# Performance work log

Measured on AMD Instinct MI355X. Metric: run time of the kernel, lower is better.

The kernel has to match this reference:

```python
import jax, jax.numpy as jnp
import numpy as np

N, E, MUL, NZ, NR = 8192, 65536, 64, 10, 8
SQ3 = 3.0 ** 0.5
SQ2 = 2.0 ** 0.5


def _mlp(x, ws):
    # e3nn FullyConnectedNet: no biases, 1/sqrt(fan_in) scaling, silu on hidden layers
    for i, w in enumerate(ws):
        x = x @ w / jnp.sqrt(jnp.float32(w.shape[0]))
        if i < len(ws) - 1:
            x = jax.nn.silu(x)
    return x


def setup_inputs() -> dict:
    key = jax.random.key(0)
    ks = jax.random.split(key, 20)
    g = lambda i, sh: jax.random.normal(ks[i], sh, dtype=jnp.float32)
    return dict(
        node_attrs=jax.random.uniform(ks[0], (N, NZ), dtype=jnp.float32),
        node_feats=g(1, (N, MUL * 4)),            # 64x0e + 64x1o
        edge_attrs=g(2, (E, 4)),                  # SH: 1x0e + 1x1o
        edge_feats=g(3, (E, NR)),                 # radial basis
        edge_index=jax.random.randint(ks[4], (2, E), 0, N),
        magmom_node_inv_feats=g(5, (N, NR)),
        magmom_node_attrs=g(6, (N, 4)),           # 1x0e + 1x1o
        W_up_s=g(7, (MUL, MUL)), W_up_v=g(8, (MUL, MUL)),
        rmlp_w0=g(9, (2 * NR, 64)), rmlp_w1=g(10, (64, 64)),
        rmlp_w2=g(11, (64, 64)), rmlp_w3=g(12, (64, 5 * MUL)),
        mag_w=g(13, (2 * NR, 13 * MUL)),
        dens_w=g(14, (NR, 1)),
        lin_s_w=g(15, (5 * MUL, MUL)), lin_v_w=g(16, (8 * MUL, MUL)),
        skip_w_s=g(17, (MUL, NZ, MUL)), skip_w_v=g(18, (MUL, NZ, MUL)),
    )


def reference(node_attrs, node_feats, edge_attrs, edge_feats, edge_index,
              magmom_node_inv_feats, magmom_node_attrs,
              W_up_s, W_up_v, rmlp_w0, rmlp_w1, rmlp_w2, rmlp_w3,
              mag_w, dens_w, lin_s_w, lin_v_w, skip_w_s, skip_w_v):
    sender, receiver = edge_index[0], edge_index[1]
    num_nodes = node_feats.shape[0]
    mul = W_up_s.shape[0]

    # linear_up (per-l channel mixing)
    s = node_feats[:, :mul]
    v = node_feats[:, mul:].reshape(num_nodes, mul, 3)
    s = (s @ W_up_s) / jnp.sqrt(jnp.float32(mul))
    v = jnp.einsum('nui,uw->nwi', v, W_up_v) / jnp.sqrt(jnp.float32(mul))

    # radial weights conditioned on edge feats + sender magmom invariants
    efm = jnp.concatenate([edge_feats, magmom_node_inv_feats[sender]], axis=-1)
    tp_w = _mlp(efm, [rmlp_w0, rmlp_w1, rmlp_w2, rmlp_w3]).reshape(-1, 5, mul)
    wm = (efm @ mag_w / jnp.sqrt(jnp.float32(mag_w.shape[0]))).reshape(-1, 13, mul)
    edge_density = jnp.tanh((edge_feats @ dens_w / jnp.sqrt(jnp.float32(NR))) ** 2)  # [E,1]

    # conv_tp: node_feats[sender] x edge SH, uvu with per-edge weights (5 paths)
    xs, xv = s[sender], v[sender]          # [E,mul], [E,mul,3]
    y0, y1 = edge_attrs[:, :1], edge_attrs[:, 1:]
    m_s0 = tp_w[:, 0] * xs * y0                                       # 0e x 0e -> 0e
    m_v0 = tp_w[:, 1, :, None] * xs[:, :, None] * y1[:, None, :]      # 0e x 1o -> 1o
    m_v1 = tp_w[:, 2, :, None] * xv * y0[:, :, None]                  # 1o x 0e -> 1o
    m_s1 = tp_w[:, 3] * jnp.einsum('eui,ei->eu', xv, y1) / SQ3        # 1o x 1o -> 0e
    m_v2 = tp_w[:, 4, :, None] * jnp.cross(xv, y1[:, None, :]) / SQ2  # 1o x 1o -> 1e

    # magmom_conv_tp: mji x magmom_node_attrs[sender], uvu (13 paths)
    ma = magmom_node_attrs[sender]
    m0, m1 = ma[:, :1], ma[:, 1:]
    out_s, out_v = [], []
    p = 0
    for ss in (m_s0, m_s1):
        out_s.append(wm[:, p] * ss * m0); p += 1
        out_v.append(wm[:, p, :, None] * ss[:, :, None] * m1[:, None, :]); p += 1
    for vv in (m_v0, m_v1, m_v2):
        out_v.append(wm[:, p, :, None] * vv * m0[:, :, None]); p += 1
        out_s.append(wm[:, p] * jnp.einsum('eui,ei->eu', vv, m1) / SQ3); p += 1
        out_v.append(wm[:, p, :, None] * jnp.cross(vv, m1[:, None, :]) / SQ2); p += 1
    mm_s = jnp.stack(out_s, axis=1)   # [E,5,mul]
    mm_v = jnp.stack(out_v, axis=1)   # [E,8,mul,3]

    # scatter-sum to receivers
    density = jax.ops.segment_sum(edge_density, receiver, num_segments=num_nodes)  # [N,1]
    ms = jax.ops.segment_sum(mm_s, receiver, num_segments=num_nodes)               # [N,5,mul]
    mv = jax.ops.segment_sum(mm_v, receiver, num_segments=num_nodes)               # [N,8,mul,3]

    # magmom_linear + density normalization
    ms = ms.reshape(num_nodes, 5 * mul) @ lin_s_w / jnp.sqrt(jnp.float32(5 * mul))
    mv = jnp.einsum('nui,uw->nwi', mv.reshape(num_nodes, 8 * mul, 3), lin_v_w) / jnp.sqrt(jnp.float32(8 * mul))
    ms = ms / (density + 1.0)
    mv = mv / (density[:, :, None] + 1.0)

    # skip FullyConnectedTensorProduct with scalar node_attrs (species one-hot)
    fan = jnp.sqrt(jnp.float32(skip_w_s.shape[0] * skip_w_s.shape[1]))
    o_s = jnp.einsum('nu,nv,uvw->nw', ms, node_attrs, skip_w_s) / fan
    o_v = jnp.einsum('nui,nv,uvw->nwi', mv, node_attrs, skip_w_v) / fan

    # reshape_irreps: [N, mul, 1+3]
    return jnp.concatenate([o_s[:, :, None], o_v], axis=-1)
```

## Files before the change

### kernel.cpp

```cpp
#include <hip/hip_runtime.h>
#include <hip/hip_bf16.h>

#define NN 8192
#define EE 65536

typedef unsigned short u16;
typedef __attribute__((ext_vector_type(8))) short bf16x8;
typedef __attribute__((ext_vector_type(8))) unsigned short u16x8;
typedef __attribute__((ext_vector_type(4))) float f32x4;

#define OFF_W0    0
#define OFF_W1    2048
#define OFF_W2    6144
#define OFF_W3M   10240
#define OFF_MAGB  59392
#define OFF_MAGC  75776
#define OFF_LINS  79872
#define OFF_LINV  100352
#define OFF_SKS   133120
#define OFF_SKV   174080
#define WT_TOTAL  215040

__device__ __forceinline__ u16 f2bf(float f) {
  __hip_bfloat16 h = __float2bfloat16(f);
  return *reinterpret_cast<u16*>(&h);
}
__device__ __forceinline__ float bf2f(u16 v) {
  union { unsigned int u; float f; } x; x.u = ((unsigned int)v) << 16; return x.f;
}
__device__ __forceinline__ void split2(float x, u16& h, u16& l) {
  __hip_bfloat16 bh = __float2bfloat16(x);
  h = *reinterpret_cast<u16*>(&bh);
  float r = x - __bfloat162float(bh);
  __hip_bfloat16 bl = __float2bfloat16(r);
  l = *reinterpret_cast<u16*>(&bl);
}

#define MFMA(a, b, c) __builtin_amdgcn_mfma_f32_16x16x32_bf16((a), (b), (c), 0, 0, 0)

__global__ __launch_bounds__(256, 4) void k_edge(
    const u16* __restrict__ efm_h, const u16* __restrict__ efm_l,
    const u16* __restrict__ wt_h, const u16* __restrict__ wt_l,
    u16* __restrict__ cmbA, u16* __restrict__ cmbB, u16* __restrict__ cmbC)
{
  __shared__ u16 Hh[64 * 72], Hl[64 * 72];
  __shared__ u16 Bs[2][3072];
  __shared__ u16 Ct[64 * 80];
  const int tid  = threadIdx.x;
  const size_t pos0 = (size_t)blockIdx.x * 64;
  const int wave = tid >> 6, lane = tid & 63;
  const int quad = lane >> 4, lrow = lane & 15;
  const int kbase = quad * 8;
  const int rw = wave * 16;

  bf16x8 eah = {}, eal = {};
  if (quad < 2) {
    eah = *reinterpret_cast<const bf16x8*>(&efm_h[(pos0 + rw + lrow) * 16 + kbase]);
    eal = *reinterpret_cast<const bf16x8*>(&efm_l[(pos0 + rw + lrow) * 16 + kbase]);
  }

  {
    #pragma unroll
    for (int nt = 0; nt < 4; ++nt) {
      const size_t bo = (size_t)nt * 512 + lane * 8;
      const bf16x8 fbh = *reinterpret_cast<const bf16x8*>(wt_h + OFF_W0 + bo);
      const bf16x8 fbl = *reinterpret_cast<const bf16x8*>(wt_l + OFF_W0 + bo);
      f32x4 acc = {};
      acc = MFMA(eah, fbh, acc); acc = MFMA(eah, fbl, acc); acc = MFMA(eal, fbh, acc);
      #pragma unroll
      for (int r = 0; r < 4; ++r) {
        float t = acc[r];
        t = t / (1.0f + __expf(-t));
        u16 hh, ll; split2(t, hh, ll);
        const int row = rw + quad * 4 + r, col = nt * 16 + lrow;
        Hh[row * 72 + col] = hh; Hl[row * 72 + col] = ll;
      }
    }
  }

  #pragma unroll
  for (int layer = 0; layer < 2; ++layer) {
    const int OFF = layer ? OFF_W2 : OFF_W1;
    bf16x8 fah[2], fal[2];
    #pragma unroll
    for (int ks = 0; ks < 2; ++ks) {
      fah[ks] = *reinterpret_cast<const bf16x8*>(&Hh[(rw + lrow) * 72 + ks * 32 + kbase]);
      fal[ks] = *reinterpret_cast<const bf16x8*>(&Hl[(rw + lrow) * 72 + ks * 32 + kbase]);
    }
    f32x4 acc[4] = {};
    #pragma unroll
    for (int nt = 0; nt < 4; ++nt)
      #pragma unroll
      for (int ks = 0; ks < 2; ++ks) {
        const size_t bo = (size_t)(nt * 2 + ks) * 512 + lane * 8;
        const bf16x8 fbh = *reinterpret_cast<const bf16x8*>(wt_h + OFF + bo);
        const bf16x8 fbl = *reinterpret_cast<const bf16x8*>(wt_l + OFF + bo);
        acc[nt] = MFMA(fah[ks], fbh, acc[nt]);
        acc[nt] = MFMA(fah[ks], fbl, acc[nt]);
        acc[nt] = MFMA(fal[ks], fbh, acc[nt]);
      }
    #pragma unroll
    for (int nt = 0; nt < 4; ++nt)
      #pragma unroll
      for (int r = 0; r < 4; ++r) {
        float t = acc[nt][r];
        t = t / (1.0f + __expf(-t));
        u16 hh, ll; split2(t, hh, ll);
        const int row = rw + quad * 4 + r, col = nt * 16 + lrow;
        Hh[row * 72 + col] = hh; Hl[row * 72 + col] = ll;
      }
  }

  {
    bf16x8 fah[3], fal[3];
    #pragma unroll
    for (int ks = 0; ks < 2; ++ks) {
      fah[ks] = *reinterpret_cast<const bf16x8*>(&Hh[(rw + lrow) * 72 + ks * 32 + kbase]);
      fal[ks] = *reinterpret_cast<const bf16x8*>(&Hl[(rw + lrow) * 72 + ks * 32 + kbase]);
    }
    fah[2] = eah; fal[2] = eal;

    auto STAGE_A = [&](int s, int buf) {
      const size_t src = (size_t)OFF_W3M + (size_t)s * 1536;
      #pragma unroll
      for (int i = 0; i < 2; ++i) {
        const int idx = tid + i * 256;
        if (idx < 384) {
          const int b = (idx >= 192);
          const int off = (idx - (b ? 192 : 0)) * 8;
          *reinterpret_cast<uint4*>(&Bs[buf][(b ? 1536 : 0) + off]) =
              *reinterpret_cast<const uint4*>((b ? wt_l : wt_h) + src + off);
        }
      }
    };

    STAGE_A(0, 0);
    for (int s = 0; s < 32; ++s) {
      __syncthreads();
      if (s + 1 < 32) STAGE_A(s + 1, (s + 1) & 1);
      const int nt = s & 3;
      f32x4 acc = {};
      #pragma unroll
      for (int ks = 0; ks < 3; ++ks) {
        const bf16x8 bh = *reinterpret_cast<const bf16x8*>(&Bs[s & 1][ks * 512 + lane * 8]);
        const bf16x8 bl = *reinterpret_cast<const bf16x8*>(&Bs[s & 1][1536 + ks * 512 + lane * 8]);
        acc = MFMA(fah[ks], bh, acc); acc = MFMA(fah[ks], bl, acc); acc = MFMA(fal[ks], bh, acc);
      }
      #pragma unroll
      for (int r = 0; r < 4; ++r)
        Ct[(rw + quad * 4 + r) * 80 + ((nt * 16 + lrow) ^ (quad << 4))] = f2bf(acc[r]);
      if (nt == 3) {
        u16* dstA = cmbA + (size_t)(s >> 2) * ((size_t)EE * 64);
        #pragma unroll
        for (int i = 0; i < 2; ++i) {
          const int idx = lane + i * 64;
          const int rl = idx >> 3, c2 = idx & 7;
          const uint4 v4 = *reinterpret_cast<const uint4*>(
              &Ct[(rw + rl) * 80 + ((c2 * 8) ^ (((rl >> 2) & 3) << 4))]);
          *reinterpret_cast<uint4*>(&dstA[(pos0 + rw + rl) * 64 + c2 * 8]) = v4;
        }
      }
    }
  }

  {
    auto STAGE_B = [&](int t, int buf) {
      const size_t src = (size_t)OFF_MAGB + (size_t)t * 512;
      if (tid < 128) {
        const int b = (tid >= 64);
        const int off = (tid - (b ? 64 : 0)) * 8;
        *reinterpret_cast<uint4*>(&Bs[buf][(b ? 1536 : 0) + off]) =
            *reinterpret_cast<const uint4*>((b ? wt_l : wt_h) + src + off);
      }
    };

    STAGE_B(0, 0);
    for (int t = 0; t < 40; ++t) {
      __syncthreads();
      if (t + 1 < 40) STAGE_B(t + 1, (t + 1) & 1);
      const int nt = t & 3;
      const bf16x8 bh = *reinterpret_cast<const bf16x8*>(&Bs[t & 1][lane * 8]);
      const bf16x8 bl = *reinterpret_cast<const bf16x8*>(&Bs[t & 1][1536 + lane * 8]);
      f32x4 acc = {};
      acc = MFMA(eah, bh, acc); acc = MFMA(eah, bl, acc); acc = MFMA(eal, bh, acc);
      #pragma unroll
      for (int r = 0; r < 4; ++r)
        Ct[(rw + quad * 4 + r) * 80 + ((nt * 16 + lrow) ^ (quad << 4))] = f2bf(acc[r]);
      if (nt == 3) {
        const int g = t >> 2;
        u16* dst = (g < 8) ? (cmbB + (size_t)g * ((size_t)EE * 64))
                           : (cmbC + (size_t)(g - 8) * ((size_t)EE * 64));
        #pragma unroll
        for (int i = 0; i < 2; ++i) {
          const int idx = lane + i * 64;
          const int rl = idx >> 3, c2 = idx & 7;
          const uint4 v4 = *reinterpret_cast<const uint4*>(
              &Ct[(rw + rl) * 80 + ((c2 * 8) ^ (((rl >> 2) & 3) << 4))]);
          *reinterpret_cast<uint4*>(&dst[(pos0 + rw + rl) * 64 + c2 * 8]) = v4;
        }
      }
    }
  }
}

template<int RT, int OUT, bool SILU, int DDIV>
__global__ __launch_bounds__(256) void k_mgemm(
    const u16* __restrict__ X1h, const u16* __restrict__ X1l, int x1rs, int K1,
    const u16* __restrict__ X2h, const u16* __restrict__ X2l, int x2rs, int K2,
    const u16* __restrict__ Wth, const u16* __restrict__ Wtl, int K,
    void* __restrict__ O1, void* __restrict__ O2, int ors,
    const float* __restrict__ dens)
{
  constexpr int NTN = (RT == 128) ? 4 : 1;
  constexpr int AIT = RT * 8 / 256;
  __shared__ u16 Ah[RT * 40];
  __shared__ u16 Al[RT * 40];
  __shared__ u16 Bh[64 * 40];
  __shared__ u16 Bl[64 * 40];
  const int tid  = threadIdx.x;
  const int row0 = blockIdx.x * RT;
  const int col0 = blockIdx.y * 64;
  const int wave = tid >> 6, lane = tid & 63;
  const int quad = lane >> 4, lrow = lane & 15;
  const int kbase = quad * 8;
  const int rw  = (RT == 128) ? wave * 32 : 0;
  const int ntb = (RT == 128) ? 0 : wave;

  f32x4 acc[2][NTN] = {};

  for (int k0 = 0; k0 < K; k0 += 32) {
    #pragma unroll
    for (int i = 0; i < AIT; ++i) {
      const int idx = tid + i * 256;
      const int b = idx / (RT * 4), rc = idx & (RT * 4 - 1);
      const int r = rc >> 2, c = rc & 3;
      const int gk = k0 + c * 8;
      uint4 v = make_uint4(0u, 0u, 0u, 0u);
      if (gk < K1)
        v = *reinterpret_cast<const uint4*>(&(b ? X1l : X1h)[(size_t)(row0 + r) * x1rs + gk]);
      else if (gk - K1 < K2)
        v = *reinterpret_cast<const uint4*>(&(b ? X2l : X2h)[(size_t)(row0 + r) * x2rs + gk - K1]);
      *reinterpret_cast<uint4*>(&(b ? Al : Ah)[r * 40 + c * 8]) = v;
    }
    #pragma unroll
    for (int i = 0; i < 2; ++i) {
      const int idx = tid + i * 256;
      const int b = idx >> 8, rc = idx & 255;
      const int n = rc >> 2, c = rc & 3;
      const uint4 v = *reinterpret_cast<const uint4*>(
          &(b ? Wtl : Wth)[(size_t)(col0 + n) * K + k0 + c * 8]);
      *reinterpret_cast<uint4*>(&(b ? Bl : Bh)[n * 40 + c * 8]) = v;
    }
    __syncthreads();

    bf16x8 fah[2], fal[2], fbh[NTN], fbl[NTN];
    #pragma unroll
    for (int mt = 0; mt < 2; ++mt) {
      const int ro = (rw + mt * 16 + lrow) * 40 + kbase;
      fah[mt] = *reinterpret_cast<const bf16x8*>(&Ah[ro]);
      fal[mt] = *reinterpret_cast<const bf16x8*>(&Al[ro]);
    }
    #pragma unroll
    for (int nt = 0; nt < NTN; ++nt) {
      const int ro = ((ntb + nt) * 16 + lrow) * 40 + kbase;
      fbh[nt] = *reinterpret_cast<const bf16x8*>(&Bh[ro]);
      fbl[nt] = *reinterpret_cast<const bf16x8*>(&Bl[ro]);
    }
    #pragma unroll
    for (int mt = 0; mt < 2; ++mt)
      #pragma unroll
      for (int nt = 0; nt < NTN; ++nt) {
        acc[mt][nt] = MFMA(fah[mt], fbh[nt], acc[mt][nt]);
        acc[mt][nt] = MFMA(fah[mt], fbl[nt], acc[mt][nt]);
        acc[mt][nt] = MFMA(fal[mt], fbh[nt], acc[mt][nt]);
      }
    __syncthreads();
  }

  #pragma unroll
  for (int mt = 0; mt < 2; ++mt)
    #pragma unroll
    for (int nt = 0; nt < NTN; ++nt)
      #pragma unroll
      for (int r = 0; r < 4; ++r) {
        const int grow = row0 + rw + mt * 16 + quad * 4 + r;
        const int gcol = col0 + (ntb + nt) * 16 + lrow;
        float t = acc[mt][nt][r];
        if (SILU) t = t / (1.0f + __expf(-t));
        if (DDIV > 0) t *= 1.0f / (dens[grow / DDIV] + 1.0f);
        const size_t oi = (size_t)grow * ors + gcol;
        if (OUT == 0) {
          reinterpret_cast<float*>(O1)[oi] = t;
        } else if (OUT == 1) {
          u16 hh, ll;
          split2(t, hh, ll);
          reinterpret_cast<u16*>(O1)[oi] = hh;
          reinterpret_cast<u16*>(O2)[oi] = ll;
        } else {
          reinterpret_cast<u16*>(O1)[oi] = f2bf(t);
        }
      }
}

__global__ __launch_bounds__(256) void k_skipm(
    const float* __restrict__ ms2, const float* __restrict__ mv2,
    const float* __restrict__ na,
    const u16* __restrict__ wt_h, const u16* __restrict__ wt_l,
    float* __restrict__ out)
{
  __shared__ u16 Ah[32 * 40];
  __shared__ u16 Al[32 * 40];
  __shared__ u16 Bh[64 * 40];
  __shared__ u16 Bl[64 * 40];
  const int tid  = threadIdx.x;
  const bool isv = blockIdx.x >= (NN / 32);
  const int row0 = (isv ? (blockIdx.x - NN / 32) : blockIdx.x) * 32;
  const float* C = isv ? mv2 : ms2;
  const u16* Bth = wt_h + (isv ? OFF_SKV : OFF_SKS);
  const u16* Btl = wt_l + (isv ? OFF_SKV : OFF_SKS);
  const int wave = tid >> 6, lane = tid & 63;
  const int quad = lane >> 4, lrow = lane & 15;
  const int kbase = quad * 8;

  f32x4 acc[2] = {};

  for (int k0 = 0; k0 < 640; k0 += 32) {
    #pragma unroll
    for (int i = 0; i < 4; ++i) {
      const int e = tid + i * 256;
      const int r = e >> 5, kk = e & 31;
      const int k = k0 + kk;
      const int u = k / 10, v = k - u * 10;
      const int row = row0 + r;
      const int n = isv ? (row / 3) : row;
      const float t = C[(size_t)row * 64 + u] * na[n * 10 + v];
      u16 hh, ll;
      split2(t, hh, ll);
      Ah[r * 40 + kk] = hh;
      Al[r * 40 + kk] = ll;
    }
    #pragma unroll
    for (int i = 0; i < 2; ++i) {
      const int idx = tid + i * 256;
      const int b = idx >> 8, rc = idx & 255;
      const int nw = rc >> 2, c = rc & 3;
      const uint4 v4 = *reinterpret_cast<const uint4*>(
          &(b ? Btl : Bth)[(size_t)nw * 640 + k0 + c * 8]);
      *reinterpret_cast<uint4*>(&(b ? Bl : Bh)[nw * 40 + c * 8]) = v4;
    }
    __syncthreads();

    bf16x8 fah[2], fal[2], fbh, fbl;
    #pragma unroll
    for (int mt = 0; mt < 2; ++mt) {
      const int ro = (mt * 16 + lrow) * 40 + kbase;
      fah[mt] = *reinterpret_cast<const bf16x8*>(&Ah[ro]);
      fal[mt] = *reinterpret_cast<const bf16x8*>(&Al[ro]);
    }
    {
      const int ro = (wave * 16 + lrow) * 40 + kbase;
      fbh = *reinterpret_cast<const bf16x8*>(&Bh[ro]);
      fbl = *reinterpret_cast<const bf16x8*>(&Bl[ro]);
    }
    #pragma unroll
    for (int mt = 0; mt < 2; ++mt) {
      acc[mt] = MFMA(fah[mt], fbh, acc[mt]);
      acc[mt] = MFMA(fah[mt], fbl, acc[mt]);
      acc[mt] = MFMA(fal[mt], fbh, acc[mt]);
    }
    __syncthreads();
  }

  #pragma unroll
  for (int mt = 0; mt < 2; ++mt)
    #pragma unroll
    for (int r = 0; r < 4; ++r) {
      const int row = row0 + mt * 16 + quad * 4 + r;
      const int w = wave * 16 + lrow;
      if (isv) {
        const int n = row / 3, i = row - n * 3;
        out[(size_t)n * 256 + w * 4 + 1 + i] = acc[mt][r];
      } else {
        out[(size_t)row * 256 + w * 4] = acc[mt][r];
      }
    }
}

template<int RT>
__global__ __launch_bounds__(256) void k_gemm(
    const float* __restrict__ X, int xrs, int xes, int xco, int xcob,
    const float* __restrict__ W, int K, int NOUT,
    float scale, float* __restrict__ OUTp, int ors, int oob)
{
  constexpr int RPT = RT / 16;
  __shared__ float Xs[RT * 65];
  __shared__ float Ws[64 * 64];
  const int tid  = threadIdx.x;
  const int row0 = blockIdx.x * RT;
  const int col0 = blockIdx.y * 64;
  const int z    = blockIdx.z;
  const int xc   = xco + z * xcob;
  const int oo   = z * oob;
  const int ci = tid & 15;
  const int ri = tid >> 4;
  float acc[RPT][4] = {};

  for (int k0 = 0; k0 < K; k0 += 64) {
    const int kc  = (K - k0 >= 64) ? 64 : (K - k0);
    const int ksh = (kc == 64) ? 6 : 4;
    for (int idx = tid; idx < kc * RT; idx += 256) {
      const int r = idx >> ksh, kk = idx & (kc - 1);
      Xs[r * 65 + kk] = X[(size_t)(row0 + r) * xrs + xc + (size_t)(k0 + kk) * xes];
    }
    for (int idx = tid; idx < (kc << 6); idx += 256) {
      const int kk = idx >> 6, c = idx & 63;
      Ws[kk * 64 + c] = W[(size_t)(k0 + kk) * NOUT + col0 + c];
    }
    __syncthreads();
    for (int kk = 0; kk < kc; ++kk) {
      const float4 wv = *reinterpret_cast<const float4*>(&Ws[kk * 64 + ci * 4]);
      #pragma unroll
      for (int j = 0; j < RPT; ++j) {
        const float x = Xs[(ri * RPT + j) * 65 + kk];
        acc[j][0] += x * wv.x; acc[j][1] += x * wv.y;
        acc[j][2] += x * wv.z; acc[j][3] += x * wv.w;
      }
    }
    __syncthreads();
  }

  #pragma unroll
  for (int j = 0; j < RPT; ++j) {
    const int row = row0 + ri * RPT + j;
    *reinterpret_cast<float4*>(OUTp + (size_t)row * ors + oo + col0 + ci * 4) =
        make_float4(acc[j][0] * scale, acc[j][1] * scale, acc[j][2] * scale, acc[j][3] * scale);
  }
}

__global__ __launch_bounds__(256) void k_count(const int* __restrict__ rcv, int* __restrict__ counts) {
  const int e = blockIdx.x * 256 + threadIdx.x;
  atomicAdd(&counts[rcv[e]], 1);
}

__global__ __launch_bounds__(1024) void k_scan(const int* __restrict__ counts,
                                               int* __restrict__ offs, int* __restrict__ cursor) {
  __shared__ int part[1024];
  const int tid = threadIdx.x;
  int local[8];
  int s = 0;
  #pragma unroll
  for (int j = 0; j < 8; ++j) { local[j] = s; s += counts[tid * 8 + j]; }
  part[tid] = s;
  __syncthreads();
  for (int off = 1; off < 1024; off <<= 1) {
    int v = 0;
    if (tid >= off) v = part[tid - off];
    __syncthreads();
    part[tid] += v;
    __syncthreads();
  }
  const int base = part[tid] - s;
  #pragma unroll
  for (int j = 0; j < 8; ++j) {
    const int o = base + local[j];
    offs[tid * 8 + j] = o;
    cursor[tid * 8 + j] = o;
  }
  if (tid == 1023) offs[NN] = part[1023];
}

__global__ __launch_bounds__(256) void k_fill(const int* __restrict__ rcv,
                                              int* __restrict__ cursor, int* __restrict__ perm) {
  const int e = blockIdx.x * 256 + threadIdx.x;
  const int pos = atomicAdd(&cursor[rcv[e]], 1);
  perm[pos] = e;
}

__global__ __launch_bounds__(256) void k_permw(
    const float* __restrict__ w0, const float* __restrict__ w1,
    const float* __restrict__ w2, const float* __restrict__ w3,
    const float* __restrict__ mag_w, const float* __restrict__ lin_s,
    const float* __restrict__ lin_v, const float* __restrict__ skip_s,
    const float* __restrict__ skip_v,
    u16* __restrict__ wt_h, u16* __restrict__ wt_l)
{
  const int id = blockIdx.x * 256 + threadIdx.x;
  float val = 0.f;
  if (id < OFF_W1) {
    const int i = id - OFF_W0;
    const int tile = i >> 9, rem = i & 511, lane = rem >> 3, e = rem & 7;
    const int quad = lane >> 4, lrow = lane & 15;
    const int n = tile * 16 + lrow, k = quad * 8 + e;
    val = (k < 16) ? w0[k * 64 + n] * 0.25f : 0.f;
  } else if (id < OFF_W2) {
    const int i = id - OFF_W1;
    const int tile = i >> 9, rem = i & 511, lane = rem >> 3, e = rem & 7;
    const int quad = lane >> 4, lrow = lane & 15;
    const int n = (tile >> 1) * 16 + lrow, k = (tile & 1) * 32 + quad * 8 + e;
    val = w1[k * 64 + n] * 0.125f;
  } else if (id < OFF_W3M) {
    const int i = id - OFF_W2;
    const int tile = i >> 9, rem = i & 511, lane = rem >> 3, e = rem & 7;
    const int quad = lane >> 4, lrow = lane & 15;
    const int n = (tile >> 1) * 16 + lrow, k = (tile & 1) * 32 + quad * 8 + e;
    val = w2[k * 64 + n] * 0.125f;
  } else if (id < OFF_MAGB) {
    const int i = id - OFF_W3M;
    const int tile = i >> 9, rem = i & 511, lane = rem >> 3, e = rem & 7;
    const int quad = lane >> 4, lrow = lane & 15;
    const int gnt = tile / 3, ks = tile - gnt * 3;
    const int n = (gnt >> 2) * 64 + (gnt & 3) * 16 + lrow;
    const int k = ks * 32 + quad * 8 + e;
    const int u = n >> 3, j = n & 7;
    if (k < 64)      val = (j < 5)  ? w3[k * 320 + j * 64 + u] * 0.125f : 0.f;
    else if (k < 80) val = (j >= 5) ? mag_w[(k - 64) * 832 + (j - 5) * 64 + u] * 0.25f : 0.f;
  } else if (id < OFF_LINS) {
    const int i = id - OFF_MAGB;
    const int tile = i >> 9, rem = i & 511, lane = rem >> 3, e = rem & 7;
    const int quad = lane >> 4, lrow = lane & 15;
    const int n = (tile >> 2) * 64 + (tile & 3) * 16 + lrow;
    const int k = quad * 8 + e;
    if (n < 512) {
      const int u = n >> 3, j = n & 7;
      val = (k < 16) ? mag_w[k * 832 + (j + 3) * 64 + u] * 0.25f : 0.f;
    } else {
      const int m = n - 512, u = m >> 1, j = m & 1;
      val = (k < 16) ? mag_w[k * 832 + (j + 11) * 64 + u] * 0.25f : 0.f;
    }
  } else if (id < OFF_LINV) {
    const int i = id - OFF_LINS, n = i / 320, k = i - n * 320;
    val = lin_s[k * 64 + n] * 0.05590169944f;
  } else if (id < OFF_SKS) {
    const int i = id - OFF_LINV, n = i >> 9, k = i & 511;
    val = lin_v[k * 64 + n] * 0.04419417382f;
  } else if (id < OFF_SKV) {
    const int i = id - OFF_SKS, w = i / 640, k = i - w * 640;
    val = skip_s[k * 64 + w] * 0.03952847075f;
  } else if (id < WT_TOTAL) {
    const int i = id - OFF_SKV, w = i / 640, k = i - w * 640;
    val = skip_v[k * 64 + w] * 0.03952847075f;
  } else {
    return;
  }
  u16 hh, ll;
  split2(val, hh, ll);
  wt_h[id] = hh;
  wt_l[id] = ll;
}

__global__ __launch_bounds__(256) void k_build(
    const int* __restrict__ perm, const int* __restrict__ snd,
    const float* __restrict__ edge_attrs, const float* __restrict__ edge_feats,
    const float* __restrict__ mm_inv, const float* __restrict__ dens_w,
    int* __restrict__ snd_perm, float* __restrict__ ya_perm,
    float* __restrict__ dq_perm, u16* __restrict__ efm_h, u16* __restrict__ efm_l)
{
  const int pos = blockIdx.x * 256 + threadIdx.x;
  const int e = perm[pos];
  const int s = snd[e];
  snd_perm[pos] = s;
  reinterpret_cast<float4*>(ya_perm)[pos] = reinterpret_cast<const float4*>(edge_attrs)[e];
  const float4 ef0 = reinterpret_cast<const float4*>(edge_feats)[e * 2];
  const float4 ef1 = reinterpret_cast<const float4*>(edge_feats)[e * 2 + 1];
  const float4 mi0 = reinterpret_cast<const float4*>(mm_inv)[s * 2];
  const float4 mi1 = reinterpret_cast<const float4*>(mm_inv)[s * 2 + 1];
  float q = ef0.x * dens_w[0] + ef0.y * dens_w[1] + ef0.z * dens_w[2] + ef0.w * dens_w[3]
          + ef1.x * dens_w[4] + ef1.y * dens_w[5] + ef1.z * dens_w[6] + ef1.w * dens_w[7];
  q *= 0.35355339059f;
  dq_perm[pos] = tanhf(q * q);
  float vals[16] = { ef0.x, ef0.y, ef0.z, ef0.w, ef1.x, ef1.y, ef1.z, ef1.w,
                     mi0.x, mi0.y, mi0.z, mi0.w, mi1.x, mi1.y, mi1.z, mi1.w };
  u16 hh[16], ll[16];
  #pragma unroll
  for (int i = 0; i < 16; ++i) split2(vals[i], hh[i], ll[i]);
  reinterpret_cast<uint4*>(&efm_h[(size_t)pos * 16])[0] = reinterpret_cast<uint4*>(hh)[0];
  reinterpret_cast<uint4*>(&efm_h[(size_t)pos * 16])[1] = reinterpret_cast<uint4*>(hh)[1];
  reinterpret_cast<uint4*>(&efm_l[(size_t)pos * 16])[0] = reinterpret_cast<uint4*>(ll)[0];
  reinterpret_cast<uint4*>(&efm_l[(size_t)pos * 16])[1] = reinterpret_cast<uint4*>(ll)[1];
}

__global__ __launch_bounds__(256) void k_gather(
    const int* __restrict__ snd_perm,
    const float* __restrict__ ya_perm,
    const float* __restrict__ dq_perm,
    const float* __restrict__ mm_attrs,
    const float* __restrict__ s_buf,
    const float* __restrict__ v_buf,
    const u16* __restrict__ cmbA,
    const u16* __restrict__ cmbB,
    const u16* __restrict__ cmbC,
    const int* __restrict__ offs,
    u16* __restrict__ ms_h, u16* __restrict__ ms_l,
    u16* __restrict__ mv_h, u16* __restrict__ mv_l,
    float* __restrict__ dens)
{
  __shared__ float red[2][30][64];
  const int tid  = threadIdx.x;
  const int lane = tid & 63;
  const int nib  = tid >> 7;
  const int half = (tid >> 6) & 1;
  const int n = blockIdx.x * 2 + nib;

  const u16* baseA = cmbA + ((size_t)(lane >> 3) * EE) * 64 + (lane & 7) * 8;
  const u16* baseB = cmbB + ((size_t)(lane >> 3) * EE) * 64 + (lane & 7) * 8;
  const u16* baseC = cmbC + ((size_t)(lane >> 5) * EE) * 64 + ((lane * 2) & 63);

  float acc_s[5] = {0.f, 0.f, 0.f, 0.f, 0.f};
  float acc_v[8][3] = {};
  float dacc = 0.f;
  const int start0 = offs[n], end0 = offs[n + 1];
  const int mid = start0 + ((end0 - start0 + 1) >> 1);
  const int start = half ? mid : start0;
  const int end   = half ? end0 : mid;

  int s_nx = 0;
  if (start < end) s_nx = snd_perm[start];
  for (int pos = start; pos < end; ++pos) {
    const int s = s_nx;
    if (pos + 1 < end) s_nx = snd_perm[pos + 1];

    const float4 ya = reinterpret_cast<const float4*>(ya_perm)[pos];
    const float4 mm = reinterpret_cast<const float4*>(mm_attrs)[s];
    dacc += dq_perm[pos];
    const float y0 = ya.x, y1x = ya.y, y1y = ya.z, y1z = ya.w;
    const float m0 = mm.x, m1x = mm.y, m1y = mm.z, m1z = mm.w;
    const float xs  = s_buf[s * 64 + lane];
    const float xvx = v_buf[(s * 3 + 0) * 64 + lane];
    const float xvy = v_buf[(s * 3 + 1) * 64 + lane];
    const float xvz = v_buf[(s * 3 + 2) * 64 + lane];

    const u16x8 ca = *reinterpret_cast<const u16x8*>(&baseA[(size_t)pos * 64]);
    const u16x8 cb = *reinterpret_cast<const u16x8*>(&baseB[(size_t)pos * 64]);
    const unsigned int cc = *reinterpret_cast<const unsigned int*>(&baseC[(size_t)pos * 64]);
    float tpv[5];
    #pragma unroll
    for (int j = 0; j < 5; ++j) tpv[j] = bf2f(ca[j]);
    float wv[13];
    #pragma unroll
    for (int p = 0; p < 3; ++p) wv[p] = bf2f(ca[5 + p]);
    #pragma unroll
    for (int p = 3; p < 11; ++p) wv[p] = bf2f(cb[p - 3]);
    wv[11] = bf2f((u16)(cc & 0xffffu));
    wv[12] = bf2f((u16)(cc >> 16));

    const float ms0  = tpv[0] * xs * y0;
    const float mv0x = tpv[1] * xs * y1x, mv0y = tpv[1] * xs * y1y, mv0z = tpv[1] * xs * y1z;
    const float mv1x = tpv[2] * xvx * y0, mv1y = tpv[2] * xvy * y0, mv1z = tpv[2] * xvz * y0;
    const float ms1  = tpv[3] * (xvx * y1x + xvy * y1y + xvz * y1z) * 0.57735026919f;
    const float crx = xvy * y1z - xvz * y1y;
    const float cry = xvz * y1x - xvx * y1z;
    const float crz = xvx * y1y - xvy * y1x;
    const float mv2x = tpv[4] * crx * 0.70710678119f;
    const float mv2y = tpv[4] * cry * 0.70710678119f;
    const float mv2z = tpv[4] * crz * 0.70710678119f;

    acc_s[0]    += wv[0] * ms0 * m0;
    acc_v[0][0] += wv[1] * ms0 * m1x; acc_v[0][1] += wv[1] * ms0 * m1y; acc_v[0][2] += wv[1] * ms0 * m1z;
    acc_s[1]    += wv[2] * ms1 * m0;
    acc_v[1][0] += wv[3] * ms1 * m1x; acc_v[1][1] += wv[3] * ms1 * m1y; acc_v[1][2] += wv[3] * ms1 * m1z;

#define VV_BLOCK(vx, vy, vz, pw, vslotA, sslot, vslotB)                                   \
    acc_v[vslotA][0] += wv[pw] * (vx) * m0;                                               \
    acc_v[vslotA][1] += wv[pw] * (vy) * m0;                                               \
    acc_v[vslotA][2] += wv[pw] * (vz) * m0;                                               \
    acc_s[sslot] += wv[pw + 1] * ((vx) * m1x + (vy) * m1y + (vz) * m1z) * 0.57735026919f; \
    {                                                                                     \
      const float ccx = (vy) * m1z - (vz) * m1y;                                          \
      const float ccy = (vz) * m1x - (vx) * m1z;                                          \
      const float ccz = (vx) * m1y - (vy) * m1x;                                          \
      acc_v[vslotB][0] += wv[pw + 2] * ccx * 0.70710678119f;                              \
      acc_v[vslotB][1] += wv[pw + 2] * ccy * 0.70710678119f;                              \
      acc_v[vslotB][2] += wv[pw + 2] * ccz * 0.70710678119f;                              \
    }

    VV_BLOCK(mv0x, mv0y, mv0z, 4, 2, 2, 3)
    VV_BLOCK(mv1x, mv1y, mv1z, 7, 4, 3, 5)
    VV_BLOCK(mv2x, mv2y, mv2z, 10, 6, 4, 7)
#undef VV_BLOCK
  }

  if (half == 1) {
    #pragma unroll
    for (int j = 0; j < 5; ++j) red[nib][j][lane] = acc_s[j];
    #pragma unroll
    for (int p = 0; p < 8; ++p)
      #pragma unroll
      for (int i = 0; i < 3; ++i) red[nib][5 + p * 3 + i][lane] = acc_v[p][i];
    red[nib][29][lane] = dacc;
  }
  __syncthreads();
  if (half == 0) {
    #pragma unroll
    for (int j = 0; j < 5; ++j) acc_s[j] += red[nib][j][lane];
    #pragma unroll
    for (int p = 0; p < 8; ++p)
      #pragma unroll
      for (int i = 0; i < 3; ++i) acc_v[p][i] += red[nib][5 + p * 3 + i][lane];
    dacc += red[nib][29][lane];

    #pragma unroll
    for (int j = 0; j < 5; ++j) {
      u16 hh, ll;
      split2(acc_s[j], hh, ll);
      ms_h[(size_t)n * 320 + j * 64 + lane] = hh;
      ms_l[(size_t)n * 320 + j * 64 + lane] = ll;
    }
    #pragma unroll
    for (int p = 0; p < 8; ++p)
      #pragma unroll
      for (int i = 0; i < 3; ++i) {
        u16 hh, ll;
        split2(acc_v[p][i], hh, ll);
        mv_h[((size_t)n * 3 + i) * 512 + p * 64 + lane] = hh;
        mv_l[((size_t)n * 3 + i) * 512 + p * 64 + lane] = ll;
      }
    if (lane == 0) dens[n] = dacc;
  }
}

extern "C" void kernel_launch(void* const* d_in, const int* in_sizes, int n_in,
                              void* d_out, int out_size, void* d_ws, size_t ws_size,
                              hipStream_t stream)
{
  const float* node_attrs = (const float*)d_in[0];
  const float* node_feats = (const float*)d_in[1];
  const float* edge_attrs = (const float*)d_in[2];
  const float* edge_feats = (const float*)d_in[3];
  const int*   edge_index = (const int*)d_in[4];
  const float* mm_inv     = (const float*)d_in[5];
  const float* mm_attrs   = (const float*)d_in[6];
  const float* W_up_s     = (const float*)d_in[7];
  const float* W_up_v     = (const float*)d_in[8];
  const float* w0         = (const float*)d_in[9];
  const float* w1         = (const float*)d_in[10];
  const float* w2         = (const float*)d_in[11];
  const float* w3         = (const float*)d_in[12];
  const float* mag_w      = (const float*)d_in[13];
  const float* dens_w     = (const float*)d_in[14];
  const float* lin_s      = (const float*)d_in[15];
  const float* lin_v      = (const float*)d_in[16];
  const float* skip_s     = (const float*)d_in[17];
  const float* skip_v     = (const float*)d_in[18];
  float* out = (float*)d_out;

  char* wp = (char*)d_ws;
  auto alloc = [&](size_t b) { char* p = wp; wp += (b + 255) & ~(size_t)255; return p; };
  float* s_buf  = (float*)alloc((size_t)NN * 64 * 4);
  float* v_buf  = (float*)alloc((size_t)NN * 192 * 4);
  float* ya_p   = (float*)alloc((size_t)EE * 4 * 4);
  float* dq_p   = (float*)alloc((size_t)EE * 4);
  int*   snd_p  = (int*)alloc((size_t)EE * 4);
  u16*   efm_h  = (u16*)alloc((size_t)EE * 16 * 2);
  u16*   efm_l  = (u16*)alloc((size_t)EE * 16 * 2);
  u16*   hA_h   = (u16*)alloc((size_t)EE * 64 * 2);
  u16*   hA_l   = (u16*)alloc((size_t)EE * 64 * 2);
  u16*   hB_h   = (u16*)alloc((size_t)EE * 64 * 2);
  u16*   hB_l   = (u16*)alloc((size_t)EE * 64 * 2);
  u16*   cmbA   = (u16*)alloc((size_t)EE * 512 * 2);
  u16*   cmbB   = (u16*)alloc((size_t)EE * 512 * 2);
  u16*   cmbC   = (u16*)alloc((size_t)EE * 128 * 2);
  u16*   mv_h   = (u16*)alloc((size_t)NN * 1536 * 2);
  u16*   mv_l   = (u16*)alloc((size_t)NN * 1536 * 2);
  float* dens   = (float*)alloc((size_t)NN * 4);
  int*   counts = (int*)alloc((size_t)NN * 4);
  int*   offs   = (int*)alloc((size_t)(NN + 1) * 4);
  int*   cursor = (int*)alloc((size_t)NN * 4);
  int*   perm   = (int*)alloc((size_t)EE * 4);
  u16*   wt_h   = (u16*)alloc((size_t)WT_TOTAL * 2);
  u16*   wt_l   = (u16*)alloc((size_t)WT_TOTAL * 2);
  u16*   ms_h   = hB_h;
  u16*   ms_l   = hB_l;
  float* ms2    = (float*)hA_h;
  float* mv2    = (float*)hA_l;

  const int* snd = edge_index;
  const int* rcv = edge_index + EE;

  hipMemsetAsync(counts, 0, (size_t)NN * 4, stream);
  k_count<<<EE / 256, 256, 0, stream>>>(rcv, counts);
  k_scan<<<1, 1024, 0, stream>>>(counts, offs, cursor);
  k_fill<<<EE / 256, 256, 0, stream>>>(rcv, cursor, perm);
  k_build<<<EE / 256, 256, 0, stream>>>(perm, snd, edge_attrs, edge_feats, mm_inv, dens_w,
                                        snd_p, ya_p, dq_p, efm_h, efm_l);
  k_permw<<<(WT_TOTAL + 255) / 256, 256, 0, stream>>>(w0, w1, w2, w3, mag_w, lin_s, lin_v,
                                                     skip_s, skip_v, wt_h, wt_l);

  k_gemm<32><<<dim3(NN / 32, 1, 1), 256, 0, stream>>>(
      node_feats, 256, 1, 0, 0, W_up_s, 64, 64, 0.125f, s_buf, 64, 0);
  k_gemm<32><<<dim3(NN / 32, 1, 3), 256, 0, stream>>>(
      node_feats, 256, 3, 64, 1, W_up_v, 64, 64, 0.125f, v_buf, 192, 64);

  k_edge<<<EE / 64, 256, 0, stream>>>(efm_h, efm_l, wt_h, wt_l, cmbA, cmbB, cmbC);

  k_gather<<<NN / 2, 256, 0, stream>>>(snd_p, ya_p, dq_p, mm_attrs,
                                       s_buf, v_buf, cmbA, cmbB, cmbC, offs,
                                       ms_h, ms_l, mv_h, mv_l, dens);

  k_mgemm<32, 0, false, 1><<<dim3(NN / 32, 1), 256, 0, stream>>>(
      ms_h, ms_l, 320, 320, nullptr, nullptr, 0, 0,
      wt_h + OFF_LINS, wt_l + OFF_LINS, 320, ms2, nullptr, 64, dens);
  k_mgemm<32, 0, false, 3><<<dim3(NN * 3 / 32, 1), 256, 0, stream>>>(
      mv_h, mv_l, 512, 512, nullptr, nullptr, 0, 0,
      wt_h + OFF_LINV, wt_l + OFF_LINV, 512, mv2, nullptr, 64, dens);

  k_skipm<<<NN / 32 + NN * 3 / 32, 256, 0, stream>>>(
      ms2, mv2, node_attrs, wt_h, wt_l, out);
}
```

Baseline: 295.4 us.

## Fold radial tp weights into magmom weights in edge kernel, store 13 planes

The edge kernel now keeps the five tensor-product radial weights in registers and multiplies them into the matching magnetic weights before writing. It emits 13 combined per-edge planes in a path-major layout instead of 18 interleaved planes. The weight permutation is reordered so columns come out path-major. This cuts the per-edge bytes written and read by the gather kernel and removes multiplies there. In exchange it fully unrolls the loops, which raises register pressure, and it rounds the weight product to bf16, which adds error.

After: 296.5 us. About the same (+0.4%).

```diff
diff --git a/kernel.cpp b/kernel.cpp
--- a/kernel.cpp
+++ b/kernel.cpp
@@ -14,7 +14,6 @@
 #define OFF_W2    6144
 #define OFF_W3M   10240
 #define OFF_MAGB  59392
-#define OFF_MAGC  75776
 #define OFF_LINS  79872
 #define OFF_LINV  100352
 #define OFF_SKS   133120
@@ -41,7 +40,7 @@
 __global__ __launch_bounds__(256, 4) void k_edge(
     const u16* __restrict__ efm_h, const u16* __restrict__ efm_l,
     const u16* __restrict__ wt_h, const u16* __restrict__ wt_l,
-    u16* __restrict__ cmbA, u16* __restrict__ cmbB, u16* __restrict__ cmbC)
+    u16* __restrict__ cmbP)
 {
   __shared__ u16 Hh[64 * 72], Hl[64 * 72];
   __shared__ u16 Bs[2][3072];
@@ -111,6 +110,19 @@
       }
   }
 
+  unsigned int tp[5][4][2];
+
+  auto STORE_P = [&](u16* dst) {
+    #pragma unroll
+    for (int i = 0; i < 2; ++i) {
+      const int idx = lane + i * 64;
+      const int rl = idx >> 3, c2 = idx & 7;
+      const uint4 v4 = *reinterpret_cast<const uint4*>(
+          &Ct[(rw + rl) * 80 + ((c2 * 8) ^ (((rl >> 2) & 3) << 4))]);
+      *reinterpret_cast<uint4*>(&dst[(pos0 + rw + rl) * 64 + c2 * 8]) = v4;
+    }
+  };
+
   {
     bf16x8 fah[3], fal[3];
     #pragma unroll
@@ -135,10 +147,11 @@
     };
 
     STAGE_A(0, 0);
+    #pragma unroll
     for (int s = 0; s < 32; ++s) {
       __syncthreads();
       if (s + 1 < 32) STAGE_A(s + 1, (s + 1) & 1);
-      const int nt = s & 3;
+      const int nt = s & 3, g = s >> 2;
       f32x4 acc = {};
       #pragma unroll
       for (int ks = 0; ks < 3; ++ks) {
@@ -146,19 +159,17 @@
         const bf16x8 bl = *reinterpret_cast<const bf16x8*>(&Bs[s & 1][1536 + ks * 512 + lane * 8]);
         acc = MFMA(fah[ks], bh, acc); acc = MFMA(fah[ks], bl, acc); acc = MFMA(fal[ks], bh, acc);
       }
-      #pragma unroll
-      for (int r = 0; r < 4; ++r)
-        Ct[(rw + quad * 4 + r) * 80 + ((nt * 16 + lrow) ^ (quad << 4))] = f2bf(acc[r]);
-      if (nt == 3) {
-        u16* dstA = cmbA + (size_t)(s >> 2) * ((size_t)EE * 64);
+      if (g < 5) {
+        tp[g][nt][0] = (unsigned)f2bf(acc[0]) | ((unsigned)f2bf(acc[1]) << 16);
+        tp[g][nt][1] = (unsigned)f2bf(acc[2]) | ((unsigned)f2bf(acc[3]) << 16);
+      } else {
+        const int q = (g == 7) ? 3 : 0;
         #pragma unroll
-        for (int i = 0; i < 2; ++i) {
-          const int idx = lane + i * 64;
-          const int rl = idx >> 3, c2 = idx & 7;
-          const uint4 v4 = *reinterpret_cast<const uint4*>(
-              &Ct[(rw + rl) * 80 + ((c2 * 8) ^ (((rl >> 2) & 3) << 4))]);
-          *reinterpret_cast<uint4*>(&dstA[(pos0 + rw + rl) * 64 + c2 * 8]) = v4;
+        for (int r = 0; r < 4; ++r) {
+          const float tv = bf2f((u16)((tp[q][nt][r >> 1] >> ((r & 1) * 16)) & 0xffffu));
+          Ct[(rw + quad * 4 + r) * 80 + ((nt * 16 + lrow) ^ (quad << 4))] = f2bf(acc[r] * tv);
         }
+        if (nt == 3) STORE_P(cmbP + (size_t)(g - 5) * ((size_t)EE * 64));
       }
     }
   }
@@ -175,30 +186,23 @@
     };
 
     STAGE_B(0, 0);
+    #pragma unroll
     for (int t = 0; t < 40; ++t) {
       __syncthreads();
       if (t + 1 < 40) STAGE_B(t + 1, (t + 1) & 1);
-      const int nt = t & 3;
+      const int nt = t & 3, p = t >> 2;
+      constexpr int QB[10] = {3, 1, 1, 1, 2, 2, 2, 4, 4, 4};
+      const int q = QB[p];
       const bf16x8 bh = *reinterpret_cast<const bf16x8*>(&Bs[t & 1][lane * 8]);
       const bf16x8 bl = *reinterpret_cast<const bf16x8*>(&Bs[t & 1][1536 + lane * 8]);
       f32x4 acc = {};
       acc = MFMA(eah, bh, acc); acc = MFMA(eah, bl, acc); acc = MFMA(eal, bh, acc);
       #pragma unroll
-      for (int r = 0; r < 4; ++r)
-        Ct[(rw + quad * 4 + r) * 80 + ((nt * 16 + lrow) ^ (quad << 4))] = f2bf(acc[r]);
-      if (nt == 3) {
-        const int g = t >> 2;
-        u16* dst = (g < 8) ? (cmbB + (size_t)g * ((size_t)EE * 64))
-                           : (cmbC + (size_t)(g - 8) * ((size_t)EE * 64));
-        #pragma unroll
-        for (int i = 0; i < 2; ++i) {
-          const int idx = lane + i * 64;
-          const int rl = idx >> 3, c2 = idx & 7;
-          const uint4 v4 = *reinterpret_cast<const uint4*>(
-              &Ct[(rw + rl) * 80 + ((c2 * 8) ^ (((rl >> 2) & 3) << 4))]);
-          *reinterpret_cast<uint4*>(&dst[(pos0 + rw + rl) * 64 + c2 * 8]) = v4;
-        }
-      }
+      for (int r = 0; r < 4; ++r) {
+        const float tv = bf2f((u16)((tp[q][nt][r >> 1] >> ((r & 1) * 16)) & 0xffffu));
+        Ct[(rw + quad * 4 + r) * 80 + ((nt * 16 + lrow) ^ (quad << 4))] = f2bf(acc[r] * tv);
+      }
+      if (nt == 3) STORE_P(cmbP + (size_t)(3 + p) * ((size_t)EE * 64));
     }
   }
 }
@@ -511,22 +515,20 @@
     const int gnt = tile / 3, ks = tile - gnt * 3;
     const int n = (gnt >> 2) * 64 + (gnt & 3) * 16 + lrow;
     const int k = ks * 32 + quad * 8 + e;
-    const int u = n >> 3, j = n & 7;
-    if (k < 64)      val = (j < 5)  ? w3[k * 320 + j * 64 + u] * 0.125f : 0.f;
-    else if (k < 80) val = (j >= 5) ? mag_w[(k - 64) * 832 + (j - 5) * 64 + u] * 0.25f : 0.f;
+    if (n < 320) {
+      val = (k < 64) ? w3[k * 320 + n] * 0.125f : 0.f;
+    } else {
+      const int p = (n - 320) >> 6, u = n & 63;
+      val = (k >= 64 && k < 80) ? mag_w[(k - 64) * 832 + p * 64 + u] * 0.25f : 0.f;
+    }
   } else if (id < OFF_LINS) {
     const int i = id - OFF_MAGB;
     const int tile = i >> 9, rem = i & 511, lane = rem >> 3, e = rem & 7;
     const int quad = lane >> 4, lrow = lane & 15;
     const int n = (tile >> 2) * 64 + (tile & 3) * 16 + lrow;
     const int k = quad * 8 + e;
-    if (n < 512) {
-      const int u = n >> 3, j = n & 7;
-      val = (k < 16) ? mag_w[k * 832 + (j + 3) * 64 + u] * 0.25f : 0.f;
-    } else {
-      const int m = n - 512, u = m >> 1, j = m & 1;
-      val = (k < 16) ? mag_w[k * 832 + (j + 11) * 64 + u] * 0.25f : 0.f;
-    }
+    const int p = n >> 6, u = n & 63;
+    val = (k < 16) ? mag_w[k * 832 + (3 + p) * 64 + u] * 0.25f : 0.f;
   } else if (id < OFF_LINV) {
     const int i = id - OFF_LINS, n = i / 320, k = i - n * 320;
     val = lin_s[k * 64 + n] * 0.05590169944f;
@@ -586,9 +588,7 @@
     const float* __restrict__ mm_attrs,
     const float* __restrict__ s_buf,
     const float* __restrict__ v_buf,
-    const u16* __restrict__ cmbA,
-    const u16* __restrict__ cmbB,
-    const u16* __restrict__ cmbC,
+    const u16* __restrict__ cmbP,
     const int* __restrict__ offs,
     u16* __restrict__ ms_h, u16* __restrict__ ms_l,
     u16* __restrict__ mv_h, u16* __restrict__ mv_l,
@@ -601,10 +601,6 @@
   const int half = (tid >> 6) & 1;
   const int n = blockIdx.x * 2 + nib;
 
-  const u16* baseA = cmbA + ((size_t)(lane >> 3) * EE) * 64 + (lane & 7) * 8;
-  const u16* baseB = cmbB + ((size_t)(lane >> 3) * EE) * 64 + (lane & 7) * 8;
-  const u16* baseC = cmbC + ((size_t)(lane >> 5) * EE) * 64 + ((lane * 2) & 63);
-
   float acc_s[5] = {0.f, 0.f, 0.f, 0.f, 0.f};
   float acc_v[8][3] = {};
   float dacc = 0.f;
@@ -629,53 +625,41 @@
     const float xvy = v_buf[(s * 3 + 1) * 64 + lane];
     const float xvz = v_buf[(s * 3 + 2) * 64 + lane];
 
-    const u16x8 ca = *reinterpret_cast<const u16x8*>(&baseA[(size_t)pos * 64]);
-    const u16x8 cb = *reinterpret_cast<const u16x8*>(&baseB[(size_t)pos * 64]);
-    const unsigned int cc = *reinterpret_cast<const unsigned int*>(&baseC[(size_t)pos * 64]);
-    float tpv[5];
-    #pragma unroll
-    for (int j = 0; j < 5; ++j) tpv[j] = bf2f(ca[j]);
-    float wv[13];
-    #pragma unroll
-    for (int p = 0; p < 3; ++p) wv[p] = bf2f(ca[5 + p]);
-    #pragma unroll
-    for (int p = 3; p < 11; ++p) wv[p] = bf2f(cb[p - 3]);
-    wv[11] = bf2f((u16)(cc & 0xffffu));
-    wv[12] = bf2f((u16)(cc >> 16));
-
-    const float ms0  = tpv[0] * xs * y0;
-    const float mv0x = tpv[1] * xs * y1x, mv0y = tpv[1] * xs * y1y, mv0z = tpv[1] * xs * y1z;
-    const float mv1x = tpv[2] * xvx * y0, mv1y = tpv[2] * xvy * y0, mv1z = tpv[2] * xvz * y0;
-    const float ms1  = tpv[3] * (xvx * y1x + xvy * y1y + xvz * y1z) * 0.57735026919f;
-    const float crx = xvy * y1z - xvz * y1y;
-    const float cry = xvz * y1x - xvx * y1z;
-    const float crz = xvx * y1y - xvy * y1x;
-    const float mv2x = tpv[4] * crx * 0.70710678119f;
-    const float mv2y = tpv[4] * cry * 0.70710678119f;
-    const float mv2z = tpv[4] * crz * 0.70710678119f;
-
-    acc_s[0]    += wv[0] * ms0 * m0;
-    acc_v[0][0] += wv[1] * ms0 * m1x; acc_v[0][1] += wv[1] * ms0 * m1y; acc_v[0][2] += wv[1] * ms0 * m1z;
-    acc_s[1]    += wv[2] * ms1 * m0;
-    acc_v[1][0] += wv[3] * ms1 * m1x; acc_v[1][1] += wv[3] * ms1 * m1y; acc_v[1][2] += wv[3] * ms1 * m1z;
-
-#define VV_BLOCK(vx, vy, vz, pw, vslotA, sslot, vslotB)                                   \
-    acc_v[vslotA][0] += wv[pw] * (vx) * m0;                                               \
-    acc_v[vslotA][1] += wv[pw] * (vy) * m0;                                               \
-    acc_v[vslotA][2] += wv[pw] * (vz) * m0;                                               \
-    acc_s[sslot] += wv[pw + 1] * ((vx) * m1x + (vy) * m1y + (vz) * m1z) * 0.57735026919f; \
+    float cp[13];
+    #pragma unroll
+    for (int p = 0; p < 13; ++p)
+      cp[p] = bf2f(cmbP[(size_t)p * ((size_t)EE * 64) + (size_t)pos * 64 + lane]);
+
+    const float gs0 = xs * y0;
+    const float gd  = (xvx * y1x + xvy * y1y + xvz * y1z) * 0.57735026919f;
+    const float g0x = xs * y1x, g0y = xs * y1y, g0z = xs * y1z;
+    const float g1x = xvx * y0, g1y = xvy * y0, g1z = xvz * y0;
+    const float g2x = (xvy * y1z - xvz * y1y) * 0.70710678119f;
+    const float g2y = (xvz * y1x - xvx * y1z) * 0.70710678119f;
+    const float g2z = (xvx * y1y - xvy * y1x) * 0.70710678119f;
+
+    acc_s[0]    += cp[0] * gs0 * m0;
+    acc_v[0][0] += cp[1] * gs0 * m1x; acc_v[0][1] += cp[1] * gs0 * m1y; acc_v[0][2] += cp[1] * gs0 * m1z;
+    acc_s[1]    += cp[2] * gd * m0;
+    acc_v[1][0] += cp[3] * gd * m1x; acc_v[1][1] += cp[3] * gd * m1y; acc_v[1][2] += cp[3] * gd * m1z;
+
+#define VV_BLOCK(vx, vy, vz, cA, cB, cC, vslotA, sslot, vslotB)                           \
+    acc_v[vslotA][0] += (cA) * (vx) * m0;                                                 \
+    acc_v[vslotA][1] += (cA) * (vy) * m0;                                                 \
+    acc_v[vslotA][2] += (cA) * (vz) * m0;                                                 \
+    acc_s[sslot] += (cB) * ((vx) * m1x + (vy) * m1y + (vz) * m1z) * 0.57735026919f;       \
     {                                                                                     \
       const float ccx = (vy) * m1z - (vz) * m1y;                                          \
       const float ccy = (vz) * m1x - (vx) * m1z;                                          \
       const float ccz = (vx) * m1y - (vy) * m1x;                                          \
-      acc_v[vslotB][0] += wv[pw + 2] * ccx * 0.70710678119f;                              \
-      acc_v[vslotB][1] += wv[pw + 2] * ccy * 0.70710678119f;                              \
-      acc_v[vslotB][2] += wv[pw + 2] * ccz * 0.70710678119f;                              \
-    }
-
-    VV_BLOCK(mv0x, mv0y, mv0z, 4, 2, 2, 3)
-    VV_BLOCK(mv1x, mv1y, mv1z, 7, 4, 3, 5)
-    VV_BLOCK(mv2x, mv2y, mv2z, 10, 6, 4, 7)
+      acc_v[vslotB][0] += (cC) * ccx * 0.70710678119f;                                    \
+      acc_v[vslotB][1] += (cC) * ccy * 0.70710678119f;                                    \
+      acc_v[vslotB][2] += (cC) * ccz * 0.70710678119f;                                    \
+    }
+
+    VV_BLOCK(g0x, g0y, g0z, cp[4], cp[5], cp[6], 2, 2, 3)
+    VV_BLOCK(g1x, g1y, g1z, cp[7], cp[8], cp[9], 4, 3, 5)
+    VV_BLOCK(g2x, g2y, g2z, cp[10], cp[11], cp[12], 6, 4, 7)
 #undef VV_BLOCK
   }
 
@@ -756,9 +740,7 @@
   u16*   hA_l   = (u16*)alloc((size_t)EE * 64 * 2);
   u16*   hB_h   = (u16*)alloc((size_t)EE * 64 * 2);
   u16*   hB_l   = (u16*)alloc((size_t)EE * 64 * 2);
-  u16*   cmbA   = (u16*)alloc((size_t)EE * 512 * 2);
-  u16*   cmbB   = (u16*)alloc((size_t)EE * 512 * 2);
-  u16*   cmbC   = (u16*)alloc((size_t)EE * 128 * 2);
+  u16*   cmbP   = (u16*)alloc((size_t)13 * EE * 64 * 2);
   u16*   mv_h   = (u16*)alloc((size_t)NN * 1536 * 2);
   u16*   mv_l   = (u16*)alloc((size_t)NN * 1536 * 2);
   float* dens   = (float*)alloc((size_t)NN * 4);
@@ -790,10 +772,10 @@
   k_gemm<32><<<dim3(NN / 32, 1, 3), 256, 0, stream>>>(
       node_feats, 256, 3, 64, 1, W_up_v, 64, 64, 0.125f, v_buf, 192, 64);
 
-  k_edge<<<EE / 64, 256, 0, stream>>>(efm_h, efm_l, wt_h, wt_l, cmbA, cmbB, cmbC);
+  k_edge<<<EE / 64, 256, 0, stream>>>(efm_h, efm_l, wt_h, wt_l, cmbP);
 
   k_gather<<<NN / 2, 256, 0, stream>>>(snd_p, ya_p, dq_p, mm_attrs,
-                                       s_buf, v_buf, cmbA, cmbB, cmbC, offs,
+                                       s_buf, v_buf, cmbP, offs,
                                        ms_h, ms_l, mv_h, mv_l, dens);
 
   k_mgemm<32, 0, false, 1><<<dim3(NN / 32, 1), 256, 0, stream>>>(
```
